# Kernel optimization log

Measured on AMD Instinct MI355X. Metric: run time of the kernel, lower is better.

## Reference

```python
import jax, jax.numpy as jnp
import numpy as np

IN_DIM = 300
MEM_DIM = 1024
DEPTH = 14  # perfect binary tree in heap order: N = 2**DEPTH - 1 = 16383 nodes


def _init_linear(key, out_dim, in_dim):
    # torch nn.Linear default init: U(-1/sqrt(in), 1/sqrt(in)) for W and b
    s = 1.0 / np.sqrt(in_dim)
    kw, kb = jax.random.split(key)
    W = jax.random.uniform(kw, (out_dim, in_dim), jnp.float32, -s, s)
    b = jax.random.uniform(kb, (out_dim,), jnp.float32, -s, s)
    return W, b


def setup_inputs() -> dict:
    key = jax.random.key(0)
    keys = jax.random.split(key, 9)
    N = 2 ** DEPTH - 1
    inp = {"embs": jax.random.normal(keys[0], (N, IN_DIM), jnp.float32)}
    gates = [("ix", IN_DIM), ("ih", MEM_DIM), ("fx", IN_DIM), ("fh", MEM_DIM),
             ("ox", IN_DIM), ("oh", MEM_DIM), ("ux", IN_DIM), ("uh", MEM_DIM)]
    for k, (name, d) in zip(keys[1:], gates):
        W, b = _init_linear(k, MEM_DIM, d)
        inp["W" + name] = W
        inp["b" + name] = b
    inp["depth"] = DEPTH
    return inp


def _lin(x, W, b):
    return x @ W.T + b


def reference(embs, Wix, bix, Wih, bih, Wfx, bfx, Wfh, bfh,
              Wox, box, Woh, boh, Wux, bux, Wuh, buh, depth):
    # Child-Sum TreeLSTM on a perfect binary tree (heap order), processed
    # bottom-up, batching all nodes of a level into single GEMMs.
    h = c = None
    for lvl in range(depth - 1, -1, -1):
        n = 2 ** lvl
        x = embs[n - 1:2 * n - 1]  # [n, in_dim], nodes of this level
        if h is None:
            # leaves: original code feeds a single zero child -> h_sum = 0
            # and f * child_c = 0 regardless of f
            hsum = jnp.zeros((n, MEM_DIM), embs.dtype)
            fc = jnp.zeros((n, MEM_DIM), embs.dtype)
        else:
            hc = h.reshape(n, 2, MEM_DIM)  # children hidden states
            cc = c.reshape(n, 2, MEM_DIM)  # children cell states
            hsum = hc.sum(axis=1)
            # per-child forget gate: sigmoid(fh(h_k) + fx(x))
            f = jax.nn.sigmoid(jnp.einsum('nkd,md->nkm', hc, Wfh) + bfh
                               + _lin(x, Wfx, bfx)[:, None, :])
            fc = (f * cc).sum(axis=1)
        i = jax.nn.sigmoid(_lin(x, Wix, bix) + _lin(hsum, Wih, bih))
        o = jax.nn.sigmoid(_lin(x, Wox, box) + _lin(hsum, Woh, boh))
        u = jnp.tanh(_lin(x, Wux, bux) + _lin(hsum, Wuh, buh))
        c = i * u + fc
        h = o * jnp.tanh(c)
    return jnp.stack([c[0], h[0]])  # root state (c, h): [2, MEM_DIM]
```

## Files before the change

kernel.cpp:

```cpp
#include <hip/hip_runtime.h>
#include <hip/hip_bf16.h>

#define IN_DIM 300
#define XDIM   320
#define MEM    1024
#define NTREE  16383

typedef _Float16 half8 __attribute__((ext_vector_type(8)));
typedef float    f32x4 __attribute__((ext_vector_type(4)));

__device__ __forceinline__ float sigf(float x) { return 1.0f / (1.0f + __expf(-x)); }
__device__ __forceinline__ float tanhfast(float x) { return 2.0f / (1.0f + __expf(-2.0f * x)) - 1.0f; }

#define GLOAD_LDS16(g, l) \
    __builtin_amdgcn_global_load_lds((const __attribute__((address_space(1))) void*)(g), \
                                     (__attribute__((address_space(3))) void*)(l), 16, 0, 0)

__global__ void pack_kernel(
    const float* __restrict__ embs,
    const float* __restrict__ Wix, const float* __restrict__ bix,
    const float* __restrict__ Wih, const float* __restrict__ bih,
    const float* __restrict__ Wfx, const float* __restrict__ bfx,
    const float* __restrict__ Wfh, const float* __restrict__ bfh,
    const float* __restrict__ Wox, const float* __restrict__ box_,
    const float* __restrict__ Woh, const float* __restrict__ boh,
    const float* __restrict__ Wux, const float* __restrict__ bux,
    const float* __restrict__ Wuh, const float* __restrict__ buh,
    _Float16* __restrict__ Wiou16, _Float16* __restrict__ Wfh16,
    _Float16* __restrict__ x16, _Float16* __restrict__ Bx)
{
    long long idx = (long long)blockIdx.x * blockDim.x + threadIdx.x;
    const long long n_wiou = 3072LL * 1024;
    const long long n_wfh  = 1024LL * 1024;
    const long long n_x    = 16384LL * XDIM;
    const long long n_bx   = 4096LL * XDIM;
    if (idx < n_wiou) {
        int m = (int)(idx >> 10), k = (int)(idx & 1023);
        int g = m >> 10, mm = m & 1023;
        const float* W = (g == 0) ? Wih : (g == 1) ? Woh : Wuh;
        Wiou16[idx] = (_Float16)W[(long long)mm * MEM + k];
        return;
    }
    idx -= n_wiou;
    if (idx < n_wfh) {
        Wfh16[idx] = (_Float16)Wfh[idx];
        return;
    }
    idx -= n_wfh;
    if (idx < n_x) {
        int node = (int)(idx / XDIM), j = (int)(idx % XDIM);
        float v = 0.f;
        if (node < NTREE) {
            if (j < IN_DIM) v = embs[(long long)node * IN_DIM + j];
            else if (j == IN_DIM) v = 1.0f;
        }
        x16[idx] = (_Float16)v;
        return;
    }
    idx -= n_x;
    if (idx < n_bx) {
        int r = (int)(idx / XDIM), j = (int)(idx % XDIM);
        int g = r >> 10, mm = r & 1023;
        const float* Wx = (g == 0) ? Wix : (g == 1) ? Wox : (g == 2) ? Wux : Wfx;
        const float* b1 = (g == 0) ? bix : (g == 1) ? box_ : (g == 2) ? bux : bfx;
        const float* b2 = (g == 0) ? bih : (g == 1) ? boh : (g == 2) ? buh : bfh;
        float v = 0.f;
        if (j < IN_DIM) v = Wx[(long long)mm * IN_DIM + j];
        else if (j == IN_DIM) v = b1[mm] + b2[mm];
        Bx[idx] = (_Float16)v;
    }
}

template<int BM, int BN, int BK>
__device__ __forceinline__ void gemm_core(
    const _Float16* __restrict__ A, int lda,
    const _Float16* __restrict__ B, int ldb, int K,
    _Float16* ldsA, _Float16* ldsB,
    f32x4 (&acc)[BM / 32][BN / 32])
{
    constexpr int FM = BM / 32, FN = BN / 32;
    constexpr int CPR = BK / 8, SWM = CPR - 1;
    constexpr int ACH = BM * BK / 2048, BCH = BN * BK / 2048;

    int tid = threadIdx.x, wave = tid >> 6, lane = tid & 63;
    int wr = (wave >> 1) * (BM / 2), wc = (wave & 1) * (BN / 2);
    int kq = (lane >> 4) * 8, rs = lane & 15;

    for (int k0 = 0; k0 < K; k0 += BK) {
#pragma unroll
        for (int j = 0; j < ACH; ++j) {
            int c = j * 256 + tid;
            int row = c / CPR;
            int s = (c ^ row) & SWM;
            GLOAD_LDS16(A + (long long)row * lda + k0 + s * 8,
                        &ldsA[(j * 256 + wave * 64) * 8]);
        }
#pragma unroll
        for (int j = 0; j < BCH; ++j) {
            int c = j * 256 + tid;
            int row = c / CPR;
            int s = (c ^ row) & SWM;
            GLOAD_LDS16(B + (long long)row * ldb + k0 + s * 8,
                        &ldsB[(j * 256 + wave * 64) * 8]);
        }
        __syncthreads();
#pragma unroll
        for (int kk = 0; kk < BK; kk += 32) {
            half8 a[FM], b[FN];
#pragma unroll
            for (int i = 0; i < FM; ++i) {
                int r = wr + i * 16 + rs;
                int s = ((kk + kq) >> 3) ^ (r & SWM);
                a[i] = *(const half8*)&ldsA[r * BK + s * 8];
            }
#pragma unroll
            for (int i = 0; i < FN; ++i) {
                int r = wc + i * 16 + rs;
                int s = ((kk + kq) >> 3) ^ (r & SWM);
                b[i] = *(const half8*)&ldsB[r * BK + s * 8];
            }
#pragma unroll
            for (int mi = 0; mi < FM; ++mi)
#pragma unroll
                for (int ni = 0; ni < FN; ++ni)
                    acc[mi][ni] = __builtin_amdgcn_mfma_f32_16x16x32_f16(a[mi], b[ni], acc[mi][ni], 0, 0, 0);
        }
        __syncthreads();
    }
}

template<int BM, int BN, int BK>
__global__ __launch_bounds__(256) void gemm_f16(
    const _Float16* __restrict__ A, int lda,
    const _Float16* __restrict__ B, int ldb,
    _Float16* __restrict__ C, int ldc, int K)
{
    __shared__ __align__(16) _Float16 ldsA[BM * BK];
    __shared__ __align__(16) _Float16 ldsB[BN * BK];
    constexpr int FM = BM / 32, FN = BN / 32;
    f32x4 acc[FM][FN] = {};
    gemm_core<BM, BN, BK>(A + (long long)blockIdx.x * BM * lda, lda,
                          B + (long long)blockIdx.y * BN * ldb, ldb, K,
                          ldsA, ldsB, acc);
    int tid = threadIdx.x, wave = tid >> 6, lane = tid & 63;
    int wr = (wave >> 1) * (BM / 2), wc = (wave & 1) * (BN / 2);
    int crb = wr + (lane >> 4) * 4, ccb = wc + (lane & 15);
    long long m0 = (long long)blockIdx.x * BM, n0 = (long long)blockIdx.y * BN;
#pragma unroll
    for (int mi = 0; mi < FM; ++mi)
#pragma unroll
        for (int i = 0; i < 4; ++i) {
            long long r = m0 + crb + mi * 16 + i;
#pragma unroll
            for (int ni = 0; ni < FN; ++ni)
                C[r * ldc + n0 + ccb + ni * 16] = (_Float16)acc[mi][ni][i];
        }
}

template<int BM1, int BM2, int BK>
__global__ __launch_bounds__(256) void gemm_level_act(
    const _Float16* __restrict__ Hsum, const _Float16* __restrict__ Hc,
    const _Float16* __restrict__ Wiou, const _Float16* __restrict__ Wf,
    const _Float16* __restrict__ Xp,
    _Float16* __restrict__ houact, _Float16* __restrict__ fact,
    int G1, int G2, int n)
{
    constexpr int BMX = (BM1 > BM2) ? BM1 : BM2;
    __shared__ __align__(16) _Float16 ldsA[BMX * BK];
    __shared__ __align__(16) _Float16 ldsB[128 * BK];
    int tid = threadIdx.x, wave = tid >> 6, lane = tid & 63;
    int bx = blockIdx.x;
    if (bx < G1 * 24) {
        int nb = bx / G1, mb = bx % G1;
        f32x4 acc[BM1 / 32][4] = {};
        gemm_core<BM1, 128, BK>(Hsum + (long long)mb * BM1 * 1024, 1024,
                                Wiou + (long long)nb * 128 * 1024, 1024, 1024,
                                ldsA, ldsB, acc);
        int gate = nb >> 3;
        int wr = (wave >> 1) * (BM1 / 2), wc = (wave & 1) * 64;
        int crb = wr + (lane >> 4) * 4, ccb = wc + (lane & 15);
#pragma unroll
        for (int mi = 0; mi < BM1 / 32; ++mi)
#pragma unroll
            for (int i = 0; i < 4; ++i) {
                long long row = mb * BM1 + crb + mi * 16 + i;
                long long node = (n - 1) + row;
#pragma unroll
                for (int ni = 0; ni < 4; ++ni) {
                    int col = nb * 128 + ccb + ni * 16;
                    float v = acc[mi][ni][i] + (float)Xp[node * 4096 + col];
                    float a = (gate == 2) ? tanhfast(v) : sigf(v);
                    houact[row * 3072 + col] = (_Float16)a;
                }
            }
    } else {
        int b2 = bx - G1 * 24;
        int nb = b2 / G2, mb = b2 % G2;
        f32x4 acc[BM2 / 32][4] = {};
        gemm_core<BM2, 128, BK>(Hc + (long long)mb * BM2 * 1024, 1024,
                                Wf + (long long)nb * 128 * 1024, 1024, 1024,
                                ldsA, ldsB, acc);
        int wr = (wave >> 1) * (BM2 / 2), wc = (wave & 1) * 64;
        int crb = wr + (lane >> 4) * 4, ccb = wc + (lane & 15);
#pragma unroll
        for (int mi = 0; mi < BM2 / 32; ++mi)
#pragma unroll
            for (int i = 0; i < 4; ++i) {
                long long row = mb * BM2 + crb + mi * 16 + i;
                long long node = (n - 1) + (row >> 1);
#pragma unroll
                for (int ni = 0; ni < 4; ++ni) {
                    int col = nb * 128 + ccb + ni * 16;
                    float v = acc[mi][ni][i] + (float)Xp[node * 4096 + 3072 + col];
                    fact[row * 1024 + col] = (_Float16)sigf(v);
                }
            }
    }
}

template<bool C16>
__global__ void combine_act(
    const _Float16* __restrict__ houact, const _Float16* __restrict__ fact,
    const void* __restrict__ cprevp,
    float* __restrict__ cout, _Float16* __restrict__ hout, _Float16* __restrict__ hsum,
    int n)
{
    int idx = blockIdx.x * blockDim.x + threadIdx.x;
    int npairs = n >> 1;
    if (idx >= npairs * 128) return;
    int r = idx >> 7, m8 = (idx & 127) * 8;
    float hs[8];
#pragma unroll
    for (int j = 0; j < 8; ++j) hs[j] = 0.f;
    for (int t = 0; t < 2; ++t) {
        int p = 2 * r + t;
        half8 vi = *(const half8*)&houact[(long long)p * 3072 + m8];
        half8 vo = *(const half8*)&houact[(long long)p * 3072 + 1024 + m8];
        half8 vu = *(const half8*)&houact[(long long)p * 3072 + 2048 + m8];
        half8 f0 = *(const half8*)&fact[(long long)(2 * p) * 1024 + m8];
        half8 f1 = *(const half8*)&fact[(long long)(2 * p + 1) * 1024 + m8];
        float c0[8], c1[8];
        if (C16) {
            const _Float16* cp = (const _Float16*)cprevp;
            half8 a = *(const half8*)&cp[(long long)(2 * p) * 1024 + m8];
            half8 b = *(const half8*)&cp[(long long)(2 * p + 1) * 1024 + m8];
#pragma unroll
            for (int j = 0; j < 8; ++j) { c0[j] = (float)a[j]; c1[j] = (float)b[j]; }
        } else {
            const float* cp = (const float*)cprevp;
            f32x4 a0 = *(const f32x4*)&cp[(long long)(2 * p) * 1024 + m8];
            f32x4 a1 = *(const f32x4*)&cp[(long long)(2 * p) * 1024 + m8 + 4];
            f32x4 b0 = *(const f32x4*)&cp[(long long)(2 * p + 1) * 1024 + m8];
            f32x4 b1 = *(const f32x4*)&cp[(long long)(2 * p + 1) * 1024 + m8 + 4];
#pragma unroll
            for (int j = 0; j < 4; ++j) { c0[j] = a0[j]; c0[j + 4] = a1[j]; c1[j] = b0[j]; c1[j + 4] = b1[j]; }
        }
        float cw[8], hw[8];
#pragma unroll
        for (int j = 0; j < 8; ++j) {
            float c = (float)vi[j] * (float)vu[j]
                    + (float)f0[j] * c0[j] + (float)f1[j] * c1[j];
            float h = (float)vo[j] * tanhfast(c);
            cw[j] = c; hw[j] = h; hs[j] += h;
        }
        f32x4 v0 = {cw[0], cw[1], cw[2], cw[3]}, v1 = {cw[4], cw[5], cw[6], cw[7]};
        *(f32x4*)&cout[(long long)p * 1024 + m8] = v0;
        *(f32x4*)&cout[(long long)p * 1024 + m8 + 4] = v1;
        half8 hv;
#pragma unroll
        for (int j = 0; j < 8; ++j) hv[j] = (_Float16)hw[j];
        *(half8*)&hout[(long long)p * 1024 + m8] = hv;
    }
    half8 sv;
#pragma unroll
    for (int j = 0; j < 8; ++j) sv[j] = (_Float16)hs[j];
    *(half8*)&hsum[(long long)r * 1024 + m8] = sv;
}

__global__ __launch_bounds__(256) void leaf_fused(
    const _Float16* __restrict__ x16, const _Float16* __restrict__ Bx,
    _Float16* __restrict__ cleaf, _Float16* __restrict__ hleaf,
    _Float16* __restrict__ hsum)
{
    constexpr int BK = 32, CPR = 4, SWM = 3;
    __shared__ __align__(16) _Float16 lA[64 * BK];
    __shared__ __align__(16) _Float16 lB[384 * BK];
    int tid = threadIdx.x, wave = tid >> 6, lane = tid & 63;
    int kq = (lane >> 4) * 8, rs = lane & 15;
    int wr = (wave >> 1) * 32, wc = (wave & 1) * 64;
    int m0 = blockIdx.x * 64, c0 = blockIdx.y * 128;
    const _Float16* A = x16 + (size_t)(8191 + m0) * XDIM;

    f32x4 acc[3][2][4] = {};
    for (int t = 0; t < 10; ++t) {
        int k0 = t * BK;
        {
            int c = tid, row = c / CPR, s = (c ^ row) & SWM;
            GLOAD_LDS16(A + (long long)row * XDIM + k0 + s * 8, &lA[(wave * 64) * 8]);
        }
#pragma unroll
        for (int j = 0; j < 6; ++j) {
            int c = j * 256 + tid;
            int row = c / CPR, s = (c ^ row) & SWM;
            int g = row >> 7, rr = row & 127;
            GLOAD_LDS16(Bx + (long long)(g * 1024 + c0 + rr) * XDIM + k0 + s * 8,
                        &lB[(j * 256 + wave * 64) * 8]);
        }
        __syncthreads();
        half8 a[2], b[3][4];
#pragma unroll
        for (int mi = 0; mi < 2; ++mi) {
            int r = wr + mi * 16 + rs;
            int s = (kq >> 3) ^ (r & SWM);
            a[mi] = *(const half8*)&lA[r * BK + s * 8];
        }
#pragma unroll
        for (int g = 0; g < 3; ++g)
#pragma unroll
            for (int nj = 0; nj < 4; ++nj) {
                int r = g * 128 + wc + nj * 16 + rs;
                int s = (kq >> 3) ^ (r & SWM);
                b[g][nj] = *(const half8*)&lB[r * BK + s * 8];
            }
#pragma unroll
        for (int g = 0; g < 3; ++g)
#pragma unroll
            for (int mi = 0; mi < 2; ++mi)
#pragma unroll
                for (int nj = 0; nj < 4; ++nj)
                    acc[g][mi][nj] = __builtin_amdgcn_mfma_f32_16x16x32_f16(a[mi], b[g][nj], acc[g][mi][nj], 0, 0, 0);
        __syncthreads();
    }
    int lrb = wr + (lane >> 4) * 4;
#pragma unroll
    for (int mi = 0; mi < 2; ++mi)
#pragma unroll
        for (int nj = 0; nj < 4; ++nj) {
            int col = c0 + wc + nj * 16 + rs;
            float hpair = 0.f;
#pragma unroll
            for (int i = 0; i < 4; ++i) {
                long long l = m0 + lrb + mi * 16 + i;
                float cc = sigf(acc[0][mi][nj][i]) * tanhfast(acc[2][mi][nj][i]);
                float hh = sigf(acc[1][mi][nj][i]) * tanhfast(cc);
                cleaf[l * 1024 + col] = (_Float16)cc;
                hleaf[l * 1024 + col] = (_Float16)hh;
                if (i & 1) hsum[(l >> 1) * 1024 + col] = (_Float16)(hpair + hh);
                else hpair = hh;
            }
        }
}

template<int BM1, int BM2, int BK>
__global__ __launch_bounds__(256) void gemm_level(
    const _Float16* __restrict__ Hsum, const _Float16* __restrict__ Hc,
    const _Float16* __restrict__ Wiou, const _Float16* __restrict__ Wf,
    _Float16* __restrict__ houpre, _Float16* __restrict__ fpre,
    int G1, int G2)
{
    constexpr int BMX = (BM1 > BM2) ? BM1 : BM2;
    __shared__ __align__(16) _Float16 ldsA[BMX * BK];
    __shared__ __align__(16) _Float16 ldsB[128 * BK];
    int tid = threadIdx.x, wave = tid >> 6, lane = tid & 63;
    int bx = blockIdx.x;
    if (bx < G1 * 24) {
        int nb = bx / G1, mb = bx % G1;
        f32x4 acc[BM1 / 32][4] = {};
        gemm_core<BM1, 128, BK>(Hsum + (long long)mb * BM1 * 1024, 1024,
                                Wiou + (long long)nb * 128 * 1024, 1024, 1024,
                                ldsA, ldsB, acc);
        int wr = (wave >> 1) * (BM1 / 2), wc = (wave & 1) * 64;
        int crb = wr + (lane >> 4) * 4, ccb = wc + (lane & 15);
#pragma unroll
        for (int mi = 0; mi < BM1 / 32; ++mi)
#pragma unroll
            for (int i = 0; i < 4; ++i) {
                long long row = mb * BM1 + crb + mi * 16 + i;
#pragma unroll
                for (int ni = 0; ni < 4; ++ni)
                    houpre[row * 3072 + nb * 128 + ccb + ni * 16] = (_Float16)acc[mi][ni][i];
            }
    } else {
        int b2 = bx - G1 * 24;
        int nb = b2 / G2, mb = b2 % G2;
        f32x4 acc[BM2 / 32][4] = {};
        gemm_core<BM2, 128, BK>(Hc + (long long)mb * BM2 * 1024, 1024,
                                Wf + (long long)nb * 128 * 1024, 1024, 1024,
                                ldsA, ldsB, acc);
        int wr = (wave >> 1) * (BM2 / 2), wc = (wave & 1) * 64;
        int crb = wr + (lane >> 4) * 4, ccb = wc + (lane & 15);
#pragma unroll
        for (int mi = 0; mi < BM2 / 32; ++mi)
#pragma unroll
            for (int i = 0; i < 4; ++i) {
                long long row = mb * BM2 + crb + mi * 16 + i;
#pragma unroll
                for (int ni = 0; ni < 4; ++ni)
                    fpre[row * 1024 + nb * 128 + ccb + ni * 16] = (_Float16)acc[mi][ni][i];
            }
    }
}

__global__ void combine_level(
    const _Float16* __restrict__ houpre, const _Float16* __restrict__ fpre,
    const float* __restrict__ cprev,
    const _Float16* __restrict__ Xp,
    float* __restrict__ cout, _Float16* __restrict__ hout, _Float16* __restrict__ hsum,
    int n, int gx0, float* __restrict__ fin)
{
    int idx = blockIdx.x * blockDim.x + threadIdx.x;
    int npairs = (n > 1) ? (n >> 1) : 1;
    if (idx >= npairs * 128) return;
    int r = idx >> 7, m8 = (idx & 127) * 8;
    float hs[8];
#pragma unroll
    for (int j = 0; j < 8; ++j) hs[j] = 0.f;
    int pmax = (n > 1) ? 2 : 1;
    for (int t = 0; t < pmax; ++t) {
        int p = 2 * r + t;
        long long node = gx0 + p;
        half8 phi = *(const half8*)&houpre[(long long)p * 3072 + m8];
        half8 pho = *(const half8*)&houpre[(long long)p * 3072 + 1024 + m8];
        half8 phu = *(const half8*)&houpre[(long long)p * 3072 + 2048 + m8];
        half8 pxi = *(const half8*)&Xp[node * 4096 + m8];
        half8 pxo = *(const half8*)&Xp[node * 4096 + 1024 + m8];
        half8 pxu = *(const half8*)&Xp[node * 4096 + 2048 + m8];
        half8 pxf = *(const half8*)&Xp[node * 4096 + 3072 + m8];
        half8 pf0 = *(const half8*)&fpre[(long long)(2 * p) * 1024 + m8];
        half8 pf1 = *(const half8*)&fpre[(long long)(2 * p + 1) * 1024 + m8];
        float cw[8], hw[8];
#pragma unroll
        for (int j = 0; j < 8; ++j) {
            float i  = sigf((float)phi[j] + (float)pxi[j]);
            float o  = sigf((float)pho[j] + (float)pxo[j]);
            float u  = tanhfast((float)phu[j] + (float)pxu[j]);
            float f0 = sigf((float)pf0[j] + (float)pxf[j]);
            float f1 = sigf((float)pf1[j] + (float)pxf[j]);
            float c = i * u + f0 * cprev[(long long)(2 * p) * 1024 + m8 + j]
                            + f1 * cprev[(long long)(2 * p + 1) * 1024 + m8 + j];
            float h = o * tanhfast(c);
            cw[j] = c; hw[j] = h; hs[j] += h;
        }
        if (fin) {
            f32x4 v0 = {cw[0], cw[1], cw[2], cw[3]}, v1 = {cw[4], cw[5], cw[6], cw[7]};
            f32x4 w0 = {hw[0], hw[1], hw[2], hw[3]}, w1 = {hw[4], hw[5], hw[6], hw[7]};
            *(f32x4*)&fin[m8] = v0;            *(f32x4*)&fin[m8 + 4] = v1;
            *(f32x4*)&fin[1024 + m8] = w0;     *(f32x4*)&fin[1024 + m8 + 4] = w1;
        } else {
            f32x4 v0 = {cw[0], cw[1], cw[2], cw[3]}, v1 = {cw[4], cw[5], cw[6], cw[7]};
            *(f32x4*)&cout[(long long)p * 1024 + m8] = v0;
            *(f32x4*)&cout[(long long)p * 1024 + m8 + 4] = v1;
            half8 hv;
#pragma unroll
            for (int j = 0; j < 8; ++j) hv[j] = (_Float16)hw[j];
            *(half8*)&hout[(long long)p * 1024 + m8] = hv;
        }
    }
    if (!fin) {
        half8 sv;
#pragma unroll
        for (int j = 0; j < 8; ++j) sv[j] = (_Float16)hs[j];
        *(half8*)&hsum[(long long)r * 1024 + m8] = sv;
    }
}

extern "C" void kernel_launch(void* const* d_in, const int* in_sizes, int n_in,
                              void* d_out, int out_size, void* d_ws, size_t ws_size,
                              hipStream_t stream)
{
    const float* embs = (const float*)d_in[0];
    const float* Wix = (const float*)d_in[1];  const float* bix = (const float*)d_in[2];
    const float* Wih = (const float*)d_in[3];  const float* bih = (const float*)d_in[4];
    const float* Wfx = (const float*)d_in[5];  const float* bfx = (const float*)d_in[6];
    const float* Wfh = (const float*)d_in[7];  const float* bfh = (const float*)d_in[8];
    const float* Wox = (const float*)d_in[9];  const float* box_ = (const float*)d_in[10];
    const float* Woh = (const float*)d_in[11]; const float* boh = (const float*)d_in[12];
    const float* Wux = (const float*)d_in[13]; const float* bux = (const float*)d_in[14];
    const float* Wuh = (const float*)d_in[15]; const float* buh = (const float*)d_in[16];

    char* p = (char*)d_ws;
    auto carve = [&](size_t bytes) -> char* {
        char* r = p; p += (bytes + 255) & ~(size_t)255; return r;
    };
    _Float16* Wiou16 = (_Float16*)carve((size_t)3072 * 1024 * 2);
    _Float16* Wfh16  = (_Float16*)carve((size_t)1024 * 1024 * 2);
    _Float16* Xp     = (_Float16*)carve((size_t)8192 * 4096 * 2);
    _Float16* houpre = (_Float16*)carve((size_t)4096 * 3072 * 2);
    _Float16* fpre   = (_Float16*)carve((size_t)8192 * 1024 * 2);
    _Float16* H_A    = (_Float16*)carve((size_t)8192 * 1024 * 2);
    _Float16* H_B    = (_Float16*)carve((size_t)4096 * 1024 * 2);
    _Float16* HsumA  = (_Float16*)carve((size_t)4096 * 1024 * 2);
    _Float16* HsumB  = (_Float16*)carve((size_t)4096 * 1024 * 2);
    _Float16* Cleaf  = (_Float16*)carve((size_t)8192 * 1024 * 2);
    float*    Cping  = (float*)carve((size_t)4096 * 1024 * 4);
    float*    Cpong  = (float*)carve((size_t)2048 * 1024 * 4);
    _Float16* x16 = fpre;
    _Float16* Bx  = fpre + (size_t)16384 * XDIM;

    {
        long long tot = 3072LL * 1024 + 1024LL * 1024 + 16384LL * XDIM + 4096LL * XDIM;
        pack_kernel<<<dim3((int)((tot + 255) / 256)), dim3(256), 0, stream>>>(
            embs, Wix, bix, Wih, bih, Wfx, bfx, Wfh, bfh,
            Wox, box_, Woh, boh, Wux, bux, Wuh, buh,
            Wiou16, Wfh16, x16, Bx);
    }

    gemm_f16<128, 128, 32><<<dim3(64, 32), dim3(256), 0, stream>>>(
        x16, XDIM, Bx, XDIM, Xp, 4096, XDIM);
    leaf_fused<<<dim3(128, 8), dim3(256), 0, stream>>>(x16, Bx, Cleaf, H_A, HsumA);

    const void* cprev = Cleaf;
    float* cbufs[2] = {Cping, Cpong};
    _Float16* hsums[2] = {HsumA, HsumB};
    int ci = 0, si = 0;
    _Float16* hcur = H_A;
    _Float16* hnext = H_B;

    for (int lvl = 12; lvl >= 9; --lvl) {
        int n = 1 << lvl;
        int G1 = n / 128, G2 = 2 * n / 128;
        if (n >= 1024)
            gemm_level_act<128, 128, 32><<<dim3(G1 * 24 + G2 * 8), dim3(256), 0, stream>>>(
                hsums[si], hcur, Wiou16, Wfh16, Xp, houpre, fpre, G1, G2, n);
        else
            gemm_level_act<128, 128, 128><<<dim3(G1 * 24 + G2 * 8), dim3(256), 0, stream>>>(
                hsums[si], hcur, Wiou16, Wfh16, Xp, houpre, fpre, G1, G2, n);
        int blocks = ((n >> 1) * 128 + 255) / 256;
        if (lvl == 12)
            combine_act<true><<<dim3(blocks), dim3(256), 0, stream>>>(
                houpre, fpre, cprev, cbufs[ci], hnext, hsums[si ^ 1], n);
        else
            combine_act<false><<<dim3(blocks), dim3(256), 0, stream>>>(
                houpre, fpre, cprev, cbufs[ci], hnext, hsums[si ^ 1], n);
        cprev = cbufs[ci];
        ci ^= 1; si ^= 1;
        _Float16* tmp = hcur; hcur = hnext; hnext = tmp;
    }

    for (int lvl = 8; lvl >= 0; --lvl) {
        int n = 1 << lvl;
        if (n >= 128) {
            int G1 = n / 128, G2 = 2 * n / 128;
            gemm_level<128, 128, 128><<<dim3(G1 * 24 + G2 * 8), dim3(256), 0, stream>>>(
                hsums[si], hcur, Wiou16, Wfh16, houpre, fpre, G1, G2);
        } else if (n == 64) {
            gemm_level<64, 128, 128><<<dim3(32), dim3(256), 0, stream>>>(
                hsums[si], hcur, Wiou16, Wfh16, houpre, fpre, 1, 1);
        } else {
            gemm_level<64, 64, 128><<<dim3(32), dim3(256), 0, stream>>>(
                hsums[si], hcur, Wiou16, Wfh16, houpre, fpre, 1, 1);
        }
        int npairs = (n > 1) ? (n >> 1) : 1;
        int blocks = (npairs * 128 + 255) / 256;
        combine_level<<<dim3(blocks), dim3(256), 0, stream>>>(
            houpre, fpre, (const float*)cprev, Xp,
            cbufs[ci], hnext, hsums[si ^ 1], n, n - 1,
            (lvl == 0) ? (float*)d_out : nullptr);
        cprev = cbufs[ci];
        ci ^= 1; si ^= 1;
        _Float16* tmp = hcur; hcur = hnext; hnext = tmp;
    }
}
```

Baseline: 487.4 us.

## Fuse GEMM and combine into single tail kernel for small tree levels

For levels 8..0, the separate gemm_level plus combine_level pair is replaced by one tail_level kernel. It multiplies each child's hidden state by all four weight groups, sums the child pair in registers, and applies the gate activations and cell update in the epilogue, so no intermediate buffers or hsum are written. The large levels go back from the activation-fused GEMM to plain gemm_level, with activations moved into a templated combine_level. The fused tail does roughly twice the i/o/u GEMM work, since it runs on both children rather than their sum, and uses only a few blocks at small n.

```diff
diff --git a/kernel.cpp b/kernel.cpp
--- a/kernel.cpp
+++ b/kernel.cpp
@@ -154,200 +154,6 @@
 #pragma unroll
             for (int ni = 0; ni < FN; ++ni)
                 C[r * ldc + n0 + ccb + ni * 16] = (_Float16)acc[mi][ni][i];
-        }
-}
-
-template<int BM1, int BM2, int BK>
-__global__ __launch_bounds__(256) void gemm_level_act(
-    const _Float16* __restrict__ Hsum, const _Float16* __restrict__ Hc,
-    const _Float16* __restrict__ Wiou, const _Float16* __restrict__ Wf,
-    const _Float16* __restrict__ Xp,
-    _Float16* __restrict__ houact, _Float16* __restrict__ fact,
-    int G1, int G2, int n)
-{
-    constexpr int BMX = (BM1 > BM2) ? BM1 : BM2;
-    __shared__ __align__(16) _Float16 ldsA[BMX * BK];
-    __shared__ __align__(16) _Float16 ldsB[128 * BK];
-    int tid = threadIdx.x, wave = tid >> 6, lane = tid & 63;
-    int bx = blockIdx.x;
-    if (bx < G1 * 24) {
-        int nb = bx / G1, mb = bx % G1;
-        f32x4 acc[BM1 / 32][4] = {};
-        gemm_core<BM1, 128, BK>(Hsum + (long long)mb * BM1 * 1024, 1024,
-                                Wiou + (long long)nb * 128 * 1024, 1024, 1024,
-                                ldsA, ldsB, acc);
-        int gate = nb >> 3;
-        int wr = (wave >> 1) * (BM1 / 2), wc = (wave & 1) * 64;
-        int crb = wr + (lane >> 4) * 4, ccb = wc + (lane & 15);
-#pragma unroll
-        for (int mi = 0; mi < BM1 / 32; ++mi)
-#pragma unroll
-            for (int i = 0; i < 4; ++i) {
-                long long row = mb * BM1 + crb + mi * 16 + i;
-                long long node = (n - 1) + row;
-#pragma unroll
-                for (int ni = 0; ni < 4; ++ni) {
-                    int col = nb * 128 + ccb + ni * 16;
-                    float v = acc[mi][ni][i] + (float)Xp[node * 4096 + col];
-                    float a = (gate == 2) ? tanhfast(v) : sigf(v);
-                    houact[row * 3072 + col] = (_Float16)a;
-                }
-            }
-    } else {
-        int b2 = bx - G1 * 24;
-        int nb = b2 / G2, mb = b2 % G2;
-        f32x4 acc[BM2 / 32][4] = {};
-        gemm_core<BM2, 128, BK>(Hc + (long long)mb * BM2 * 1024, 1024,
-                                Wf + (long long)nb * 128 * 1024, 1024, 1024,
-                                ldsA, ldsB, acc);
-        int wr = (wave >> 1) * (BM2 / 2), wc = (wave & 1) * 64;
-        int crb = wr + (lane >> 4) * 4, ccb = wc + (lane & 15);
-#pragma unroll
-        for (int mi = 0; mi < BM2 / 32; ++mi)
-#pragma unroll
-            for (int i = 0; i < 4; ++i) {
-                long long row = mb * BM2 + crb + mi * 16 + i;
-                long long node = (n - 1) + (row >> 1);
-#pragma unroll
-                for (int ni = 0; ni < 4; ++ni) {
-                    int col = nb * 128 + ccb + ni * 16;
-                    float v = acc[mi][ni][i] + (float)Xp[node * 4096 + 3072 + col];
-                    fact[row * 1024 + col] = (_Float16)sigf(v);
-                }
-            }
-    }
-}
-
-template<bool C16>
-__global__ void combine_act(
-    const _Float16* __restrict__ houact, const _Float16* __restrict__ fact,
-    const void* __restrict__ cprevp,
-    float* __restrict__ cout, _Float16* __restrict__ hout, _Float16* __restrict__ hsum,
-    int n)
-{
-    int idx = blockIdx.x * blockDim.x + threadIdx.x;
-    int npairs = n >> 1;
-    if (idx >= npairs * 128) return;
-    int r = idx >> 7, m8 = (idx & 127) * 8;
-    float hs[8];
-#pragma unroll
-    for (int j = 0; j < 8; ++j) hs[j] = 0.f;
-    for (int t = 0; t < 2; ++t) {
-        int p = 2 * r + t;
-        half8 vi = *(const half8*)&houact[(long long)p * 3072 + m8];
-        half8 vo = *(const half8*)&houact[(long long)p * 3072 + 1024 + m8];
-        half8 vu = *(const half8*)&houact[(long long)p * 3072 + 2048 + m8];
-        half8 f0 = *(const half8*)&fact[(long long)(2 * p) * 1024 + m8];
-        half8 f1 = *(const half8*)&fact[(long long)(2 * p + 1) * 1024 + m8];
-        float c0[8], c1[8];
-        if (C16) {
-            const _Float16* cp = (const _Float16*)cprevp;
-            half8 a = *(const half8*)&cp[(long long)(2 * p) * 1024 + m8];
-            half8 b = *(const half8*)&cp[(long long)(2 * p + 1) * 1024 + m8];
-#pragma unroll
-            for (int j = 0; j < 8; ++j) { c0[j] = (float)a[j]; c1[j] = (float)b[j]; }
-        } else {
-            const float* cp = (const float*)cprevp;
-            f32x4 a0 = *(const f32x4*)&cp[(long long)(2 * p) * 1024 + m8];
-            f32x4 a1 = *(const f32x4*)&cp[(long long)(2 * p) * 1024 + m8 + 4];
-            f32x4 b0 = *(const f32x4*)&cp[(long long)(2 * p + 1) * 1024 + m8];
-            f32x4 b1 = *(const f32x4*)&cp[(long long)(2 * p + 1) * 1024 + m8 + 4];
-#pragma unroll
-            for (int j = 0; j < 4; ++j) { c0[j] = a0[j]; c0[j + 4] = a1[j]; c1[j] = b0[j]; c1[j + 4] = b1[j]; }
-        }
-        float cw[8], hw[8];
-#pragma unroll
-        for (int j = 0; j < 8; ++j) {
-            float c = (float)vi[j] * (float)vu[j]
-                    + (float)f0[j] * c0[j] + (float)f1[j] * c1[j];
-            float h = (float)vo[j] * tanhfast(c);
-            cw[j] = c; hw[j] = h; hs[j] += h;
-        }
-        f32x4 v0 = {cw[0], cw[1], cw[2], cw[3]}, v1 = {cw[4], cw[5], cw[6], cw[7]};
-        *(f32x4*)&cout[(long long)p * 1024 + m8] = v0;
-        *(f32x4*)&cout[(long long)p * 1024 + m8 + 4] = v1;
-        half8 hv;
-#pragma unroll
-        for (int j = 0; j < 8; ++j) hv[j] = (_Float16)hw[j];
-        *(half8*)&hout[(long long)p * 1024 + m8] = hv;
-    }
-    half8 sv;
-#pragma unroll
-    for (int j = 0; j < 8; ++j) sv[j] = (_Float16)hs[j];
-    *(half8*)&hsum[(long long)r * 1024 + m8] = sv;
-}
-
-__global__ __launch_bounds__(256) void leaf_fused(
-    const _Float16* __restrict__ x16, const _Float16* __restrict__ Bx,
-    _Float16* __restrict__ cleaf, _Float16* __restrict__ hleaf,
-    _Float16* __restrict__ hsum)
-{
-    constexpr int BK = 32, CPR = 4, SWM = 3;
-    __shared__ __align__(16) _Float16 lA[64 * BK];
-    __shared__ __align__(16) _Float16 lB[384 * BK];
-    int tid = threadIdx.x, wave = tid >> 6, lane = tid & 63;
-    int kq = (lane >> 4) * 8, rs = lane & 15;
-    int wr = (wave >> 1) * 32, wc = (wave & 1) * 64;
-    int m0 = blockIdx.x * 64, c0 = blockIdx.y * 128;
-    const _Float16* A = x16 + (size_t)(8191 + m0) * XDIM;
-
-    f32x4 acc[3][2][4] = {};
-    for (int t = 0; t < 10; ++t) {
-        int k0 = t * BK;
-        {
-            int c = tid, row = c / CPR, s = (c ^ row) & SWM;
-            GLOAD_LDS16(A + (long long)row * XDIM + k0 + s * 8, &lA[(wave * 64) * 8]);
-        }
-#pragma unroll
-        for (int j = 0; j < 6; ++j) {
-            int c = j * 256 + tid;
-            int row = c / CPR, s = (c ^ row) & SWM;
-            int g = row >> 7, rr = row & 127;
-            GLOAD_LDS16(Bx + (long long)(g * 1024 + c0 + rr) * XDIM + k0 + s * 8,
-                        &lB[(j * 256 + wave * 64) * 8]);
-        }
-        __syncthreads();
-        half8 a[2], b[3][4];
-#pragma unroll
-        for (int mi = 0; mi < 2; ++mi) {
-            int r = wr + mi * 16 + rs;
-            int s = (kq >> 3) ^ (r & SWM);
-            a[mi] = *(const half8*)&lA[r * BK + s * 8];
-        }
-#pragma unroll
-        for (int g = 0; g < 3; ++g)
-#pragma unroll
-            for (int nj = 0; nj < 4; ++nj) {
-                int r = g * 128 + wc + nj * 16 + rs;
-                int s = (kq >> 3) ^ (r & SWM);
-                b[g][nj] = *(const half8*)&lB[r * BK + s * 8];
-            }
-#pragma unroll
-        for (int g = 0; g < 3; ++g)
-#pragma unroll
-            for (int mi = 0; mi < 2; ++mi)
-#pragma unroll
-                for (int nj = 0; nj < 4; ++nj)
-                    acc[g][mi][nj] = __builtin_amdgcn_mfma_f32_16x16x32_f16(a[mi], b[g][nj], acc[g][mi][nj], 0, 0, 0);
-        __syncthreads();
-    }
-    int lrb = wr + (lane >> 4) * 4;
-#pragma unroll
-    for (int mi = 0; mi < 2; ++mi)
-#pragma unroll
-        for (int nj = 0; nj < 4; ++nj) {
-            int col = c0 + wc + nj * 16 + rs;
-            float hpair = 0.f;
-#pragma unroll
-            for (int i = 0; i < 4; ++i) {
-                long long l = m0 + lrb + mi * 16 + i;
-                float cc = sigf(acc[0][mi][nj][i]) * tanhfast(acc[2][mi][nj][i]);
-                float hh = sigf(acc[1][mi][nj][i]) * tanhfast(cc);
-                cleaf[l * 1024 + col] = (_Float16)cc;
-                hleaf[l * 1024 + col] = (_Float16)hh;
-                if (i & 1) hsum[(l >> 1) * 1024 + col] = (_Float16)(hpair + hh);
-                else hpair = hh;
-            }
         }
 }
 
@@ -401,22 +207,22 @@
     }
 }
 
+template<bool C16>
 __global__ void combine_level(
     const _Float16* __restrict__ houpre, const _Float16* __restrict__ fpre,
-    const float* __restrict__ cprev,
+    const void* __restrict__ cprevp,
     const _Float16* __restrict__ Xp,
     float* __restrict__ cout, _Float16* __restrict__ hout, _Float16* __restrict__ hsum,
-    int n, int gx0, float* __restrict__ fin)
+    int n, int gx0)
 {
     int idx = blockIdx.x * blockDim.x + threadIdx.x;
-    int npairs = (n > 1) ? (n >> 1) : 1;
+    int npairs = n >> 1;
     if (idx >= npairs * 128) return;
     int r = idx >> 7, m8 = (idx & 127) * 8;
     float hs[8];
 #pragma unroll
     for (int j = 0; j < 8; ++j) hs[j] = 0.f;
-    int pmax = (n > 1) ? 2 : 1;
-    for (int t = 0; t < pmax; ++t) {
+    for (int t = 0; t < 2; ++t) {
         int p = 2 * r + t;
         long long node = gx0 + p;
         half8 phi = *(const half8*)&houpre[(long long)p * 3072 + m8];
@@ -428,6 +234,22 @@
         half8 pxf = *(const half8*)&Xp[node * 4096 + 3072 + m8];
         half8 pf0 = *(const half8*)&fpre[(long long)(2 * p) * 1024 + m8];
         half8 pf1 = *(const half8*)&fpre[(long long)(2 * p + 1) * 1024 + m8];
+        float c0[8], c1[8];
+        if (C16) {
+            const _Float16* cp = (const _Float16*)cprevp;
+            half8 a = *(const half8*)&cp[(long long)(2 * p) * 1024 + m8];
+            half8 b = *(const half8*)&cp[(long long)(2 * p + 1) * 1024 + m8];
+#pragma unroll
+            for (int j = 0; j < 8; ++j) { c0[j] = (float)a[j]; c1[j] = (float)b[j]; }
+        } else {
+            const float* cp = (const float*)cprevp;
+            f32x4 a0 = *(const f32x4*)&cp[(long long)(2 * p) * 1024 + m8];
+            f32x4 a1 = *(const f32x4*)&cp[(long long)(2 * p) * 1024 + m8 + 4];
+            f32x4 b0 = *(const f32x4*)&cp[(long long)(2 * p + 1) * 1024 + m8];
+            f32x4 b1 = *(const f32x4*)&cp[(long long)(2 * p + 1) * 1024 + m8 + 4];
+#pragma unroll
+            for (int j = 0; j < 4; ++j) { c0[j] = a0[j]; c0[j + 4] = a1[j]; c1[j] = b0[j]; c1[j + 4] = b1[j]; }
+        }
         float cw[8], hw[8];
 #pragma unroll
         for (int j = 0; j < 8; ++j) {
@@ -436,32 +258,197 @@
             float u  = tanhfast((float)phu[j] + (float)pxu[j]);
             float f0 = sigf((float)pf0[j] + (float)pxf[j]);
             float f1 = sigf((float)pf1[j] + (float)pxf[j]);
-            float c = i * u + f0 * cprev[(long long)(2 * p) * 1024 + m8 + j]
-                            + f1 * cprev[(long long)(2 * p + 1) * 1024 + m8 + j];
+            float c = i * u + f0 * c0[j] + f1 * c1[j];
             float h = o * tanhfast(c);
             cw[j] = c; hw[j] = h; hs[j] += h;
         }
-        if (fin) {
-            f32x4 v0 = {cw[0], cw[1], cw[2], cw[3]}, v1 = {cw[4], cw[5], cw[6], cw[7]};
-            f32x4 w0 = {hw[0], hw[1], hw[2], hw[3]}, w1 = {hw[4], hw[5], hw[6], hw[7]};
-            *(f32x4*)&fin[m8] = v0;            *(f32x4*)&fin[m8 + 4] = v1;
-            *(f32x4*)&fin[1024 + m8] = w0;     *(f32x4*)&fin[1024 + m8 + 4] = w1;
-        } else {
-            f32x4 v0 = {cw[0], cw[1], cw[2], cw[3]}, v1 = {cw[4], cw[5], cw[6], cw[7]};
-            *(f32x4*)&cout[(long long)p * 1024 + m8] = v0;
-            *(f32x4*)&cout[(long long)p * 1024 + m8 + 4] = v1;
-            half8 hv;
-#pragma unroll
-            for (int j = 0; j < 8; ++j) hv[j] = (_Float16)hw[j];
-            *(half8*)&hout[(long long)p * 1024 + m8] = hv;
-        }
-    }
-    if (!fin) {
-        half8 sv;
-#pragma unroll
-        for (int j = 0; j < 8; ++j) sv[j] = (_Float16)hs[j];
-        *(half8*)&hsum[(long long)r * 1024 + m8] = sv;
-    }
+        f32x4 v0 = {cw[0], cw[1], cw[2], cw[3]}, v1 = {cw[4], cw[5], cw[6], cw[7]};
+        *(f32x4*)&cout[(long long)p * 1024 + m8] = v0;
+        *(f32x4*)&cout[(long long)p * 1024 + m8 + 4] = v1;
+        half8 hv;
+#pragma unroll
+        for (int j = 0; j < 8; ++j) hv[j] = (_Float16)hw[j];
+        *(half8*)&hout[(long long)p * 1024 + m8] = hv;
+    }
+    half8 sv;
+#pragma unroll
+    for (int j = 0; j < 8; ++j) sv[j] = (_Float16)hs[j];
+    *(half8*)&hsum[(long long)r * 1024 + m8] = sv;
+}
+
+__global__ __launch_bounds__(256) void leaf_fused(
+    const _Float16* __restrict__ x16, const _Float16* __restrict__ Bx,
+    _Float16* __restrict__ cleaf, _Float16* __restrict__ hleaf,
+    _Float16* __restrict__ hsum)
+{
+    constexpr int BK = 32, CPR = 4, SWM = 3;
+    __shared__ __align__(16) _Float16 lA[64 * BK];
+    __shared__ __align__(16) _Float16 lB[384 * BK];
+    int tid = threadIdx.x, wave = tid >> 6, lane = tid & 63;
+    int kq = (lane >> 4) * 8, rs = lane & 15;
+    int wr = (wave >> 1) * 32, wc = (wave & 1) * 64;
+    int m0 = blockIdx.x * 64, c0 = blockIdx.y * 128;
+    const _Float16* A = x16 + (size_t)(8191 + m0) * XDIM;
+
+    f32x4 acc[3][2][4] = {};
+    for (int t = 0; t < 10; ++t) {
+        int k0 = t * BK;
+        {
+            int c = tid, row = c / CPR, s = (c ^ row) & SWM;
+            GLOAD_LDS16(A + (long long)row * XDIM + k0 + s * 8, &lA[(wave * 64) * 8]);
+        }
+#pragma unroll
+        for (int j = 0; j < 6; ++j) {
+            int c = j * 256 + tid;
+            int row = c / CPR, s = (c ^ row) & SWM;
+            int g = row >> 7, rr = row & 127;
+            GLOAD_LDS16(Bx + (long long)(g * 1024 + c0 + rr) * XDIM + k0 + s * 8,
+                        &lB[(j * 256 + wave * 64) * 8]);
+        }
+        __syncthreads();
+        half8 a[2], b[3][4];
+#pragma unroll
+        for (int mi = 0; mi < 2; ++mi) {
+            int r = wr + mi * 16 + rs;
+            int s = (kq >> 3) ^ (r & SWM);
+            a[mi] = *(const half8*)&lA[r * BK + s * 8];
+        }
+#pragma unroll
+        for (int g = 0; g < 3; ++g)
+#pragma unroll
+            for (int nj = 0; nj < 4; ++nj) {
+                int r = g * 128 + wc + nj * 16 + rs;
+                int s = (kq >> 3) ^ (r & SWM);
+                b[g][nj] = *(const half8*)&lB[r * BK + s * 8];
+            }
+#pragma unroll
+        for (int g = 0; g < 3; ++g)
+#pragma unroll
+            for (int mi = 0; mi < 2; ++mi)
+#pragma unroll
+                for (int nj = 0; nj < 4; ++nj)
+                    acc[g][mi][nj] = __builtin_amdgcn_mfma_f32_16x16x32_f16(a[mi], b[g][nj], acc[g][mi][nj], 0, 0, 0);
+        __syncthreads();
+    }
+    int lrb = wr + (lane >> 4) * 4;
+#pragma unroll
+    for (int mi = 0; mi < 2; ++mi)
+#pragma unroll
+        for (int nj = 0; nj < 4; ++nj) {
+            int col = c0 + wc + nj * 16 + rs;
+            float hpair = 0.f;
+#pragma unroll
+            for (int i = 0; i < 4; ++i) {
+                long long l = m0 + lrb + mi * 16 + i;
+                float cc = sigf(acc[0][mi][nj][i]) * tanhfast(acc[2][mi][nj][i]);
+                float hh = sigf(acc[1][mi][nj][i]) * tanhfast(cc);
+                cleaf[l * 1024 + col] = (_Float16)cc;
+                hleaf[l * 1024 + col] = (_Float16)hh;
+                if (i & 1) hsum[(l >> 1) * 1024 + col] = (_Float16)(hpair + hh);
+                else hpair = hh;
+            }
+        }
+}
+
+__global__ __launch_bounds__(256, 1) void tail_level(
+    const _Float16* __restrict__ Hc,
+    const _Float16* __restrict__ Wiou, const _Float16* __restrict__ Wf,
+    const float* __restrict__ cprev,
+    const _Float16* __restrict__ Xp,
+    float* __restrict__ cout, _Float16* __restrict__ hout,
+    int n, int PT, float* __restrict__ fin)
+{
+    constexpr int BK = 128, CPR = 16, SWM = 15;
+    __shared__ __align__(16) _Float16 lA[128 * BK];
+    __shared__ __align__(16) _Float16 lB[256 * BK];
+    int tid = threadIdx.x, wave = tid >> 6, lane = tid & 63;
+    int kq = (lane >> 4) * 8, rs = lane & 15;
+    int p0 = ((int)blockIdx.x % PT) * 64, c0 = ((int)blockIdx.x / PT) * 64;
+    int wr = (wave >> 1) * 64, wc = (wave & 1) * 32;
+
+    f32x4 acc[4][4][2] = {};
+    for (int t = 0; t < 8; ++t) {
+        int k0 = t * BK;
+#pragma unroll
+        for (int j = 0; j < 8; ++j) {
+            int c = j * 256 + tid;
+            int row = c / CPR;
+            int s = (c ^ row) & SWM;
+            GLOAD_LDS16(Hc + (long long)(2 * p0 + row) * 1024 + k0 + s * 8,
+                        &lA[(j * 256 + wave * 64) * 8]);
+        }
+#pragma unroll
+        for (int j = 0; j < 16; ++j) {
+            int c = j * 256 + tid;
+            int row = c / CPR;
+            int s = (c ^ row) & SWM;
+            int g = row >> 6, rr = row & 63;
+            const _Float16* src = (g < 3)
+                ? (Wiou + (long long)(g * 1024 + c0 + rr) * 1024)
+                : (Wf + (long long)(c0 + rr) * 1024);
+            GLOAD_LDS16(src + k0 + s * 8, &lB[(j * 256 + wave * 64) * 8]);
+        }
+        __syncthreads();
+#pragma unroll
+        for (int kk = 0; kk < BK; kk += 32) {
+            half8 a[4], b[4][2];
+#pragma unroll
+            for (int mi = 0; mi < 4; ++mi) {
+                int r = wr + mi * 16 + rs;
+                int s = ((kk + kq) >> 3) ^ (r & SWM);
+                a[mi] = *(const half8*)&lA[r * BK + s * 8];
+            }
+#pragma unroll
+            for (int g = 0; g < 4; ++g)
+#pragma unroll
+                for (int nj = 0; nj < 2; ++nj) {
+                    int r = g * 64 + wc + nj * 16 + rs;
+                    int s = ((kk + kq) >> 3) ^ (r & SWM);
+                    b[g][nj] = *(const half8*)&lB[r * BK + s * 8];
+                }
+#pragma unroll
+            for (int g = 0; g < 4; ++g)
+#pragma unroll
+                for (int mi = 0; mi < 4; ++mi)
+#pragma unroll
+                    for (int nj = 0; nj < 2; ++nj)
+                        acc[g][mi][nj] = __builtin_amdgcn_mfma_f32_16x16x32_f16(a[mi], b[g][nj], acc[g][mi][nj], 0, 0, 0);
+        }
+        __syncthreads();
+    }
+    int lrb = wr + (lane >> 4) * 4;
+#pragma unroll
+    for (int mi = 0; mi < 4; ++mi)
+#pragma unroll
+        for (int nj = 0; nj < 2; ++nj) {
+            int col = c0 + wc + nj * 16 + rs;
+#pragma unroll
+            for (int ii = 0; ii < 2; ++ii) {
+                int ca = lrb + mi * 16 + 2 * ii;
+                int p = p0 + (ca >> 1);
+                if (p >= n) continue;
+                long long node = (n - 1) + p;
+                float pi = acc[0][mi][nj][2 * ii] + acc[0][mi][nj][2 * ii + 1]
+                         + (float)Xp[node * 4096 + col];
+                float po = acc[1][mi][nj][2 * ii] + acc[1][mi][nj][2 * ii + 1]
+                         + (float)Xp[node * 4096 + 1024 + col];
+                float pu = acc[2][mi][nj][2 * ii] + acc[2][mi][nj][2 * ii + 1]
+                         + (float)Xp[node * 4096 + 2048 + col];
+                float xf = (float)Xp[node * 4096 + 3072 + col];
+                float f0 = sigf(acc[3][mi][nj][2 * ii] + xf);
+                float f1 = sigf(acc[3][mi][nj][2 * ii + 1] + xf);
+                float c = sigf(pi) * tanhfast(pu)
+                        + f0 * cprev[(long long)(2 * p) * 1024 + col]
+                        + f1 * cprev[(long long)(2 * p + 1) * 1024 + col];
+                float h = sigf(po) * tanhfast(c);
+                if (fin) {
+                    if (p == 0) { fin[col] = c; fin[1024 + col] = h; }
+                } else {
+                    cout[(long long)p * 1024 + col] = c;
+                    hout[(long long)p * 1024 + col] = (_Float16)h;
+                }
+            }
+        }
 }
 
 extern "C" void kernel_launch(void* const* d_in, const int* in_sizes, int n_in,
@@ -519,19 +506,15 @@
     for (int lvl = 12; lvl >= 9; --lvl) {
         int n = 1 << lvl;
         int G1 = n / 128, G2 = 2 * n / 128;
-        if (n >= 1024)
-            gemm_level_act<128, 128, 32><<<dim3(G1 * 24 + G2 * 8), dim3(256), 0, stream>>>(
-                hsums[si], hcur, Wiou16, Wfh16, Xp, houpre, fpre, G1, G2, n);
-        else
-            gemm_level_act<128, 128, 128><<<dim3(G1 * 24 + G2 * 8), dim3(256), 0, stream>>>(
-                hsums[si], hcur, Wiou16, Wfh16, Xp, houpre, fpre, G1, G2, n);
+        gemm_level<128, 128, 32><<<dim3(G1 * 24 + G2 * 8), dim3(256), 0, stream>>>(
+            hsums[si], hcur, Wiou16, Wfh16, houpre, fpre, G1, G2);
         int blocks = ((n >> 1) * 128 + 255) / 256;
         if (lvl == 12)
-            combine_act<true><<<dim3(blocks), dim3(256), 0, stream>>>(
-                houpre, fpre, cprev, cbufs[ci], hnext, hsums[si ^ 1], n);
+            combine_level<true><<<dim3(blocks), dim3(256), 0, stream>>>(
+                houpre, fpre, cprev, Xp, cbufs[ci], hnext, hsums[si ^ 1], n, n - 1);
         else
-            combine_act<false><<<dim3(blocks), dim3(256), 0, stream>>>(
-                houpre, fpre, cprev, cbufs[ci], hnext, hsums[si ^ 1], n);
+            combine_level<false><<<dim3(blocks), dim3(256), 0, stream>>>(
+                houpre, fpre, cprev, Xp, cbufs[ci], hnext, hsums[si ^ 1], n, n - 1);
         cprev = cbufs[ci];
         ci ^= 1; si ^= 1;
         _Float16* tmp = hcur; hcur = hnext; hnext = tmp;
@@ -539,25 +522,13 @@
 
     for (int lvl = 8; lvl >= 0; --lvl) {
         int n = 1 << lvl;
-        if (n >= 128) {
-            int G1 = n / 128, G2 = 2 * n / 128;
-            gemm_level<128, 128, 128><<<dim3(G1 * 24 + G2 * 8), dim3(256), 0, stream>>>(
-                hsums[si], hcur, Wiou16, Wfh16, houpre, fpre, G1, G2);
-        } else if (n == 64) {
-            gemm_level<64, 128, 128><<<dim3(32), dim3(256), 0, stream>>>(
-                hsums[si], hcur, Wiou16, Wfh16, houpre, fpre, 1, 1);
-        } else {
-            gemm_level<64, 64, 128><<<dim3(32), dim3(256), 0, stream>>>(
-                hsums[si], hcur, Wiou16, Wfh16, houpre, fpre, 1, 1);
-        }
-        int npairs = (n > 1) ? (n >> 1) : 1;
-        int blocks = (npairs * 128 + 255) / 256;
-        combine_level<<<dim3(blocks), dim3(256), 0, stream>>>(
-            houpre, fpre, (const float*)cprev, Xp,
-            cbufs[ci], hnext, hsums[si ^ 1], n, n - 1,
+        int PT = (n + 63) >> 6;
+        tail_level<<<dim3(PT * 16), dim3(256), 0, stream>>>(
+            hcur, Wiou16, Wfh16, (const float*)cprev, Xp,
+            cbufs[ci], hnext, n, PT,
             (lvl == 0) ? (float*)d_out : nullptr);
         cprev = cbufs[ci];
-        ci ^= 1; si ^= 1;
+        ci ^= 1;
         _Float16* tmp = hcur; hcur = hnext; hnext = tmp;
     }
 }
```

Result: slower. 554.8 us (+13.8%).
